# Kernel tuning notes

Hardware: AMD Instinct MI355X
Metric: run time of the kernel (lower is better)

Reference implementation:

```python
import jax, jax.numpy as jnp
import numpy as np

N_NODES = 50000
N_EDGES = 800000
N_GRAPHS = 256
DIMS = [64, 128, 256, 512]
GRU_H = 256


def _linit(key, shape, fan_in):
    lim = 1.0 / np.sqrt(fan_in)
    return jax.random.uniform(key, shape, jnp.float32, -lim, lim)


def setup_inputs() -> dict:
    key = jax.random.key(0)
    ks = jax.random.split(key, 24)
    x = jax.random.normal(ks[0], (N_NODES, DIMS[0]), jnp.float32)
    edge_index = jax.random.randint(ks[1], (2, N_EDGES), 0, N_NODES, jnp.int64)
    batch_idx = jnp.sort(jax.random.randint(ks[2], (N_NODES,), 0, N_GRAPHS, jnp.int64))
    inp = {"x": x, "edge_index": edge_index, "batch_idx": batch_idx}
    # GCN layer weights (stored [in, out]) and biases
    for i in range(3):
        inp[f"gcn_w{i}"] = _linit(ks[3 + i], (DIMS[i], DIMS[i + 1]), DIMS[i])
        inp[f"gcn_b{i}"] = jnp.zeros((DIMS[i + 1],), jnp.float32)
    # gate nn: Linear(512, 1)
    inp["gate_w"] = _linit(ks[6], (DIMS[3], 1), DIMS[3])
    inp["gate_b"] = jnp.zeros((1,), jnp.float32)
    # GRU: 2 layers, torch layout W_ih [3H, in], W_hh [3H, H]
    ins = [DIMS[3], GRU_H]
    for l in range(2):
        inp[f"gru_wih{l}"] = _linit(ks[7 + 4 * l], (3 * GRU_H, ins[l]), GRU_H)
        inp[f"gru_whh{l}"] = _linit(ks[8 + 4 * l], (3 * GRU_H, GRU_H), GRU_H)
        inp[f"gru_bih{l}"] = _linit(ks[9 + 4 * l], (3 * GRU_H,), GRU_H)
        inp[f"gru_bhh{l}"] = _linit(ks[10 + 4 * l], (3 * GRU_H,), GRU_H)
    # output proj: Linear(256, 512), torch layout [out, in]
    inp["proj_w"] = _linit(ks[15], (DIMS[3], GRU_H), GRU_H)
    inp["proj_b"] = jnp.zeros((DIMS[3],), jnp.float32)
    return inp


def _gcn_norm(edge_index, n_nodes):
    # add self-loops, symmetric normalization (PyG GCNConv default)
    loop = jnp.arange(n_nodes, dtype=edge_index.dtype)
    src = jnp.concatenate([edge_index[0], loop])
    dst = jnp.concatenate([edge_index[1], loop])
    deg = jax.ops.segment_sum(jnp.ones_like(dst, jnp.float32), dst, num_segments=n_nodes)
    dinv = jnp.where(deg > 0, jax.lax.rsqrt(jnp.maximum(deg, 1.0)), 0.0)
    norm = dinv[src] * dinv[dst]
    return src, dst, norm


def _gru_cell(xv, h, wih, whh, bih, bhh):
    gi = xv @ wih.T + bih
    gh = h @ whh.T + bhh
    ir, iz, inn = jnp.split(gi, 3, axis=-1)
    hr, hz, hn = jnp.split(gh, 3, axis=-1)
    r = jax.nn.sigmoid(ir + hr)
    z = jax.nn.sigmoid(iz + hz)
    n = jnp.tanh(inn + r * hn)
    return (1.0 - z) * n + z * h


def reference(x, edge_index, batch_idx,
              gcn_w0, gcn_b0, gcn_w1, gcn_b1, gcn_w2, gcn_b2,
              gate_w, gate_b,
              gru_wih0, gru_whh0, gru_bih0, gru_bhh0,
              gru_wih1, gru_whh1, gru_bih1, gru_bhh1,
              proj_w, proj_b):
    n = x.shape[0]
    src, dst, norm = _gcn_norm(edge_index, n)
    for w, b in ((gcn_w0, gcn_b0), (gcn_w1, gcn_b1), (gcn_w2, gcn_b2)):
        h = x @ w                                  # [N, out]
        msg = h[src] * norm[:, None]               # gather over edges
        x = jax.ops.segment_sum(msg, dst, num_segments=n) + b
        x = jax.nn.relu(x)
    # attentional aggregation: segment softmax over gate scores
    gate = (x @ gate_w + gate_b)[:, 0]             # [N]
    gmax = jax.ops.segment_max(gate, batch_idx, num_segments=N_GRAPHS)
    e = jnp.exp(gate - gmax[batch_idx])
    denom = jax.ops.segment_sum(e, batch_idx, num_segments=N_GRAPHS)
    alpha = e / denom[batch_idx]
    graph_emb = jax.ops.segment_sum(x * alpha[:, None], batch_idx, num_segments=N_GRAPHS)  # [G, 512]
    # 2-layer GRU with seq_len=1, h0=0
    h0 = jnp.zeros((N_GRAPHS, GRU_H), x.dtype)
    h1 = _gru_cell(graph_emb, h0, gru_wih0, gru_whh0, gru_bih0, gru_bhh0)
    h2 = _gru_cell(h1, h0, gru_wih1, gru_whh1, gru_bih1, gru_bhh1)
    return h2 @ proj_w.T + proj_b                  # [G, 512]
```

## Files before the change

kernel.cpp:

```cpp
#include <hip/hip_runtime.h>


#define N_GRAPHS 256
#define GRU_H 256
#define SCAN_CHUNK 2048

typedef __attribute__((ext_vector_type(8))) short short8;
typedef __attribute__((ext_vector_type(4))) float floatx4;

typedef unsigned short ushort_t;
typedef unsigned int uint_t;

__device__ __forceinline__ float bflo(uint_t u) { return __uint_as_float(u << 16); }
__device__ __forceinline__ float bfhi(uint_t u) { return __uint_as_float(u & 0xffff0000u); }
__device__ __forceinline__ uint_t f2bf(float f) {
    uint_t u = __float_as_uint(f);
    return (u + 0x7fffu + ((u >> 16) & 1u)) >> 16;
}
__device__ __forceinline__ uint_t pack2(float a, float b) {
    return f2bf(a) | (f2bf(b) << 16);
}


__global__ void k_hist(const int* __restrict__ dst, int* __restrict__ counts, int E) {
    int e = blockIdx.x * blockDim.x + threadIdx.x;
    if (e < E) atomicAdd(&counts[dst[e]], 1);
}

__global__ __launch_bounds__(256) void k_scan1(const int* __restrict__ counts,
                                               int* __restrict__ rowptr,
                                               int* __restrict__ bsums,
                                               float* __restrict__ dinv, int n) {
    int b = blockIdx.x, t = threadIdx.x;
    int base = b * SCAN_CHUNK + t * 8;
    int v[8];
    int s = 0;
#pragma unroll
    for (int j = 0; j < 8; ++j) {
        int i = base + j;
        int c = (i < n) ? counts[i] : 0;
        v[j] = s;
        s += c;
        if (i < n) dinv[i] = rsqrtf((float)(c + 1));
    }
    __shared__ int sd[256];
    sd[t] = s;
    __syncthreads();
    for (int off = 1; off < 256; off <<= 1) {
        int tmp = (t >= off) ? sd[t - off] : 0;
        __syncthreads();
        sd[t] += tmp;
        __syncthreads();
    }
    int texcl = sd[t] - s;
    if (t == 255) bsums[b] = sd[255];
#pragma unroll
    for (int j = 0; j < 8; ++j) {
        int i = base + j;
        if (i < n) rowptr[i] = texcl + v[j];
    }
}

__global__ void k_scan2(int* __restrict__ bsums, int nb, int* __restrict__ rowptr, int n) {
    if (threadIdx.x == 0 && blockIdx.x == 0) {
        int run = 0;
        for (int b = 0; b < nb; ++b) { int t = bsums[b]; bsums[b] = run; run += t; }
        rowptr[n] = run;
    }
}

__global__ __launch_bounds__(256) void k_scan3(int* __restrict__ rowptr,
                                               int* __restrict__ cursor,
                                               const int* __restrict__ bsums, int n) {
    int b = blockIdx.x, t = threadIdx.x;
    int base = b * SCAN_CHUNK + t * 8;
    int off = bsums[b];
#pragma unroll
    for (int j = 0; j < 8; ++j) {
        int i = base + j;
        if (i < n) { int r = rowptr[i] + off; rowptr[i] = r; cursor[i] = r; }
    }
}

__global__ void k_fill(const int* __restrict__ src, const int* __restrict__ dst,
                       int* __restrict__ cursor, int* __restrict__ col, int E) {
    int e = blockIdx.x * blockDim.x + threadIdx.x;
    if (e < E) {
        int pos = atomicAdd(&cursor[dst[e]], 1);
        col[pos] = src[e];
    }
}


__global__ void k_wt(const float* __restrict__ W, ushort_t* __restrict__ Wt,
                     int K, int Nout, int shift ) {
    int idx = blockIdx.x * blockDim.x + threadIdx.x;
    if (idx >= K * Nout) return;
    int k = idx >> shift;
    int n = idx & (Nout - 1);
    Wt[(size_t)n * K + k] = (ushort_t)f2bf(W[idx]);
}


__global__ void k_split(const float* __restrict__ src, ushort_t* __restrict__ hi,
                        ushort_t* __restrict__ lo, int L) {
    int i = blockIdx.x * blockDim.x + threadIdx.x;
    if (i >= L) return;
    float v = src[i];
    uint_t h = f2bf(v);
    hi[i] = (ushort_t)h;
    lo[i] = (ushort_t)f2bf(v - __uint_as_float(h << 16));
}


__global__ void k_prescale(const float4* __restrict__ x, const float* __restrict__ dinv,
                           uint4* __restrict__ xs, int N) {
    int idx = blockIdx.x * blockDim.x + threadIdx.x;
    int n = idx >> 3;
    if (n >= N) return;
    float dn = dinv[n];
    float4 v0 = x[idx * 2], v1 = x[idx * 2 + 1];
    uint4 o;
    o.x = pack2(v0.x * dn, v0.y * dn);
    o.y = pack2(v0.z * dn, v0.w * dn);
    o.z = pack2(v1.x * dn, v1.y * dn);
    o.w = pack2(v1.z * dn, v1.w * dn);
    xs[idx] = o;
}


__global__ void k_gather_bf16(const uint4* __restrict__ xs, const int* __restrict__ rp,
                              const int* __restrict__ col, const float* __restrict__ dinv,
                              uint4* __restrict__ agg, int N, int shift ) {
    int idx = blockIdx.x * blockDim.x + threadIdx.x;
    int n = idx >> shift;
    if (n >= N) return;
    int c = idx & ((1 << shift) - 1);
    int C8 = 1 << shift;
    int a = rp[n], b = rp[n + 1];
    uint4 u = xs[(size_t)n * C8 + c];
    float a0 = bflo(u.x), a1 = bfhi(u.x), a2 = bflo(u.y), a3 = bfhi(u.y);
    float a4 = bflo(u.z), a5 = bfhi(u.z), a6 = bflo(u.w), a7 = bfhi(u.w);
    for (int k = a; k < b; ++k) {
        uint4 v = xs[(size_t)col[k] * C8 + c];
        a0 += bflo(v.x); a1 += bfhi(v.x); a2 += bflo(v.y); a3 += bfhi(v.y);
        a4 += bflo(v.z); a5 += bfhi(v.z); a6 += bflo(v.w); a7 += bfhi(v.w);
    }
    float dn = dinv[n];
    uint4 o;
    o.x = pack2(a0 * dn, a1 * dn);
    o.y = pack2(a2 * dn, a3 * dn);
    o.z = pack2(a4 * dn, a5 * dn);
    o.w = pack2(a6 * dn, a7 * dn);
    agg[idx] = o;
}


__global__ __launch_bounds__(256) void k_gemm_mfma(
    const ushort_t* __restrict__ A, const ushort_t* __restrict__ Wt,
    const float* __restrict__ bias, const float* __restrict__ dinv,
    ushort_t* __restrict__ C, int M, int K, int Nout, int scale_out) {
    __shared__ ushort_t As[64 * 72];
    __shared__ ushort_t Bs[64 * 72];
    int tid = threadIdx.x;
    int wave = tid >> 6, lane = tid & 63;
    int quad = lane >> 4, lr = lane & 15;
    int wm = (wave & 1) * 32, wn = (wave >> 1) * 32;
    int bm = blockIdx.x * 64, bn = blockIdx.y * 64;

    floatx4 zero = {0.f, 0.f, 0.f, 0.f};
    floatx4 acc00 = zero, acc01 = zero, acc10 = zero, acc11 = zero;

    int r0 = tid >> 3,         ko0 = (tid & 7) * 8;
    int r1 = (tid + 256) >> 3, ko1 = ((tid + 256) & 7) * 8;

    for (int k0 = 0; k0 < K; k0 += 64) {
        int ar0 = min(bm + r0, M - 1);
        int ar1 = min(bm + r1, M - 1);
        uint4 av0 = *(const uint4*)(A + (size_t)ar0 * K + k0 + ko0);
        uint4 av1 = *(const uint4*)(A + (size_t)ar1 * K + k0 + ko1);
        uint4 bv0 = *(const uint4*)(Wt + (size_t)(bn + r0) * K + k0 + ko0);
        uint4 bv1 = *(const uint4*)(Wt + (size_t)(bn + r1) * K + k0 + ko1);
        __syncthreads();
        *(uint4*)&As[r0 * 72 + ko0] = av0;
        *(uint4*)&As[r1 * 72 + ko1] = av1;
        *(uint4*)&Bs[r0 * 72 + ko0] = bv0;
        *(uint4*)&Bs[r1 * 72 + ko1] = bv1;
        __syncthreads();
#pragma unroll
        for (int ks = 0; ks < 2; ++ks) {
            short8 af0 = *(short8*)&As[(wm + lr) * 72 + ks * 32 + quad * 8];
            short8 af1 = *(short8*)&As[(wm + 16 + lr) * 72 + ks * 32 + quad * 8];
            short8 bf0 = *(short8*)&Bs[(wn + lr) * 72 + ks * 32 + quad * 8];
            short8 bf1 = *(short8*)&Bs[(wn + 16 + lr) * 72 + ks * 32 + quad * 8];
            acc00 = __builtin_amdgcn_mfma_f32_16x16x32_bf16(af0, bf0, acc00, 0, 0, 0);
            acc01 = __builtin_amdgcn_mfma_f32_16x16x32_bf16(af0, bf1, acc01, 0, 0, 0);
            acc10 = __builtin_amdgcn_mfma_f32_16x16x32_bf16(af1, bf0, acc10, 0, 0, 0);
            acc11 = __builtin_amdgcn_mfma_f32_16x16x32_bf16(af1, bf1, acc11, 0, 0, 0);
        }
    }

#pragma unroll
    for (int mi = 0; mi < 2; ++mi) {
#pragma unroll
        for (int ni = 0; ni < 2; ++ni) {
            floatx4 acc = (mi == 0) ? (ni == 0 ? acc00 : acc01)
                                    : (ni == 0 ? acc10 : acc11);
            int col = bn + wn + ni * 16 + lr;
            float bcol = bias[col];
#pragma unroll
            for (int r = 0; r < 4; ++r) {
                int row = bm + wm + mi * 16 + quad * 4 + r;
                if (row < M) {
                    float v = acc[r] + bcol;
                    v = fmaxf(v, 0.0f);
                    if (scale_out) v *= dinv[row];
                    C[(size_t)row * Nout + col] = (ushort_t)f2bf(v);
                }
            }
        }
    }
}


__global__ __launch_bounds__(256) void k_gemm3(
    const ushort_t* __restrict__ Ahi, const ushort_t* __restrict__ Alo,
    const ushort_t* __restrict__ Whi, const ushort_t* __restrict__ Wlo,
    const float* __restrict__ bias, float* __restrict__ C,
    int M, int K, int Nout) {
    __shared__ ushort_t AsH[64 * 72];
    __shared__ ushort_t AsL[64 * 72];
    __shared__ ushort_t BsH[64 * 72];
    __shared__ ushort_t BsL[64 * 72];
    int tid = threadIdx.x;
    int wave = tid >> 6, lane = tid & 63;
    int quad = lane >> 4, lr = lane & 15;
    int wm = (wave & 1) * 32, wn = (wave >> 1) * 32;
    int bm = blockIdx.x * 64, bn = blockIdx.y * 64;

    floatx4 zero = {0.f, 0.f, 0.f, 0.f};
    floatx4 acc00 = zero, acc01 = zero, acc10 = zero, acc11 = zero;

    int r0 = tid >> 3,         ko0 = (tid & 7) * 8;
    int r1 = (tid + 256) >> 3, ko1 = ((tid + 256) & 7) * 8;

    for (int k0 = 0; k0 < K; k0 += 64) {
        int ar0 = min(bm + r0, M - 1);
        int ar1 = min(bm + r1, M - 1);
        size_t a0o = (size_t)ar0 * K + k0 + ko0, a1o = (size_t)ar1 * K + k0 + ko1;
        size_t b0o = (size_t)(bn + r0) * K + k0 + ko0, b1o = (size_t)(bn + r1) * K + k0 + ko1;
        uint4 ah0 = *(const uint4*)(Ahi + a0o), ah1 = *(const uint4*)(Ahi + a1o);
        uint4 al0 = *(const uint4*)(Alo + a0o), al1 = *(const uint4*)(Alo + a1o);
        uint4 bh0 = *(const uint4*)(Whi + b0o), bh1 = *(const uint4*)(Whi + b1o);
        uint4 bl0 = *(const uint4*)(Wlo + b0o), bl1 = *(const uint4*)(Wlo + b1o);
        __syncthreads();
        *(uint4*)&AsH[r0 * 72 + ko0] = ah0; *(uint4*)&AsH[r1 * 72 + ko1] = ah1;
        *(uint4*)&AsL[r0 * 72 + ko0] = al0; *(uint4*)&AsL[r1 * 72 + ko1] = al1;
        *(uint4*)&BsH[r0 * 72 + ko0] = bh0; *(uint4*)&BsH[r1 * 72 + ko1] = bh1;
        *(uint4*)&BsL[r0 * 72 + ko0] = bl0; *(uint4*)&BsL[r1 * 72 + ko1] = bl1;
        __syncthreads();
#pragma unroll
        for (int ks = 0; ks < 2; ++ks) {
            int a0i = (wm + lr) * 72 + ks * 32 + quad * 8;
            int a1i = (wm + 16 + lr) * 72 + ks * 32 + quad * 8;
            int b0i = (wn + lr) * 72 + ks * 32 + quad * 8;
            int b1i = (wn + 16 + lr) * 72 + ks * 32 + quad * 8;
            short8 afh0 = *(short8*)&AsH[a0i], afh1 = *(short8*)&AsH[a1i];
            short8 afl0 = *(short8*)&AsL[a0i], afl1 = *(short8*)&AsL[a1i];
            short8 bfh0 = *(short8*)&BsH[b0i], bfh1 = *(short8*)&BsH[b1i];
            short8 bfl0 = *(short8*)&BsL[b0i], bfl1 = *(short8*)&BsL[b1i];
            acc00 = __builtin_amdgcn_mfma_f32_16x16x32_bf16(afh0, bfh0, acc00, 0, 0, 0);
            acc00 = __builtin_amdgcn_mfma_f32_16x16x32_bf16(afh0, bfl0, acc00, 0, 0, 0);
            acc00 = __builtin_amdgcn_mfma_f32_16x16x32_bf16(afl0, bfh0, acc00, 0, 0, 0);
            acc01 = __builtin_amdgcn_mfma_f32_16x16x32_bf16(afh0, bfh1, acc01, 0, 0, 0);
            acc01 = __builtin_amdgcn_mfma_f32_16x16x32_bf16(afh0, bfl1, acc01, 0, 0, 0);
            acc01 = __builtin_amdgcn_mfma_f32_16x16x32_bf16(afl0, bfh1, acc01, 0, 0, 0);
            acc10 = __builtin_amdgcn_mfma_f32_16x16x32_bf16(afh1, bfh0, acc10, 0, 0, 0);
            acc10 = __builtin_amdgcn_mfma_f32_16x16x32_bf16(afh1, bfl0, acc10, 0, 0, 0);
            acc10 = __builtin_amdgcn_mfma_f32_16x16x32_bf16(afl1, bfh0, acc10, 0, 0, 0);
            acc11 = __builtin_amdgcn_mfma_f32_16x16x32_bf16(afh1, bfh1, acc11, 0, 0, 0);
            acc11 = __builtin_amdgcn_mfma_f32_16x16x32_bf16(afh1, bfl1, acc11, 0, 0, 0);
            acc11 = __builtin_amdgcn_mfma_f32_16x16x32_bf16(afl1, bfh1, acc11, 0, 0, 0);
        }
    }

#pragma unroll
    for (int mi = 0; mi < 2; ++mi) {
#pragma unroll
        for (int ni = 0; ni < 2; ++ni) {
            floatx4 acc = (mi == 0) ? (ni == 0 ? acc00 : acc01)
                                    : (ni == 0 ? acc10 : acc11);
            int col = bn + wn + ni * 16 + lr;
            float bcol = bias ? bias[col] : 0.0f;
#pragma unroll
            for (int r = 0; r < 4; ++r) {
                int row = bm + wm + mi * 16 + quad * 4 + r;
                if (row < M)
                    C[(size_t)row * Nout + col] = acc[r] + bcol;
            }
        }
    }
}


__global__ void k_gru_ep(const float* __restrict__ gi, const float* __restrict__ bih,
                         const float* __restrict__ bhh,
                         ushort_t* __restrict__ hhi, ushort_t* __restrict__ hlo, int G) {
    int idx = blockIdx.x * blockDim.x + threadIdx.x;
    int g = idx >> 8, j = idx & 255;
    if (g >= G) return;
    const float* row = gi + (size_t)g * 768;
    float ir = row[j]       + bih[j]       + bhh[j];
    float iz = row[j + 256] + bih[j + 256] + bhh[j + 256];
    float in = row[j + 512] + bih[j + 512];
    float r = 1.0f / (1.0f + expf(-ir));
    float z = 1.0f / (1.0f + expf(-iz));
    float nn = tanhf(in + r * bhh[j + 512]);
    float h = (1.0f - z) * nn;
    uint_t hi = f2bf(h);
    hhi[idx] = (ushort_t)hi;
    hlo[idx] = (ushort_t)f2bf(h - __uint_as_float(hi << 16));
}


__global__ void k_gate(const uint4* __restrict__ x, const float4* __restrict__ gw,
                       const float* __restrict__ gb, float* __restrict__ gate, int N) {
    int gid = blockIdx.x * blockDim.x + threadIdx.x;
    int wave = gid >> 6;
    int lane = gid & 63;
    if (wave >= N) return;
    uint4 u = x[(size_t)wave * 64 + lane];
    float4 w0 = gw[lane * 2], w1 = gw[lane * 2 + 1];
    float acc = bflo(u.x) * w0.x + bfhi(u.x) * w0.y + bflo(u.y) * w0.z + bfhi(u.y) * w0.w
              + bflo(u.z) * w1.x + bfhi(u.z) * w1.y + bflo(u.w) * w1.z + bfhi(u.w) * w1.w;
#pragma unroll
    for (int off = 32; off > 0; off >>= 1) acc += __shfl_down(acc, off, 64);
    if (lane == 0) gate[wave] = acc + gb[0];
}


__global__ void k_gstart(const int* __restrict__ batch, int* __restrict__ gstart,
                         int N, int G) {
    int g = blockIdx.x * blockDim.x + threadIdx.x;
    if (g > G) return;
    if (g == G) { gstart[G] = N; return; }
    int lo = 0, hi = N;
    while (lo < hi) {
        int mid = (lo + hi) >> 1;
        if (batch[mid] < g) lo = mid + 1; else hi = mid;
    }
    gstart[g] = lo;
}


__global__ __launch_bounds__(256) void k_softmax_emb(
    const uint_t* __restrict__ x , const float* __restrict__ gate,
    const int* __restrict__ gstart, float* __restrict__ emb) {
    int g = blockIdx.x;
    int s = gstart[g], e = gstart[g + 1];
    __shared__ float red[256];
    __shared__ float sal[256];
    int tid = threadIdx.x;
    float m = -INFINITY;
    for (int i = s + tid; i < e; i += 256) m = fmaxf(m, gate[i]);
    red[tid] = m; __syncthreads();
    for (int off = 128; off > 0; off >>= 1) {
        if (tid < off) red[tid] = fmaxf(red[tid], red[tid + off]);
        __syncthreads();
    }
    m = red[0]; __syncthreads();
    float ssum = 0.f;
    for (int i = s + tid; i < e; i += 256) ssum += expf(gate[i] - m);
    red[tid] = ssum; __syncthreads();
    for (int off = 128; off > 0; off >>= 1) {
        if (tid < off) red[tid] += red[tid + off];
        __syncthreads();
    }
    float denom = red[0];
    float inv = (denom > 0.f) ? 1.0f / denom : 0.0f;
    float acc0 = 0.f, acc1 = 0.f;
    for (int base = s; base < e; base += 256) {
        int i = base + tid;
        __syncthreads();
        sal[tid] = (i < e) ? expf(gate[i] - m) * inv : 0.0f;
        __syncthreads();
        int cnt = min(256, e - base);
        for (int k = 0; k < cnt; ++k) {
            float a = sal[k];
            uint_t u = x[(size_t)(base + k) * 256 + tid];
            acc0 += a * bflo(u);
            acc1 += a * bfhi(u);
        }
    }
    emb[(size_t)g * 512 + tid * 2]     = acc0;
    emb[(size_t)g * 512 + tid * 2 + 1] = acc1;
}


extern "C" void kernel_launch(void* const* d_in, const int* in_sizes, int n_in,
                              void* d_out, int out_size, void* d_ws, size_t ws_size,
                              hipStream_t stream) {
    const float* x       = (const float*)d_in[0];
    const int*   ei      = (const int*)d_in[1];
    const int*   batch   = (const int*)d_in[2];
    const float* w0      = (const float*)d_in[3];
    const float* b0      = (const float*)d_in[4];
    const float* w1      = (const float*)d_in[5];
    const float* b1      = (const float*)d_in[6];
    const float* w2      = (const float*)d_in[7];
    const float* b2      = (const float*)d_in[8];
    const float* gate_w  = (const float*)d_in[9];
    const float* gate_b  = (const float*)d_in[10];
    const float* wih0    = (const float*)d_in[11];
    const float* bih0    = (const float*)d_in[13];
    const float* bhh0    = (const float*)d_in[14];
    const float* wih1    = (const float*)d_in[15];
    const float* bih1    = (const float*)d_in[17];
    const float* bhh1    = (const float*)d_in[18];
    const float* pw      = (const float*)d_in[19];
    const float* pb      = (const float*)d_in[20];
    float* out = (float*)d_out;

    const int N = in_sizes[2];
    const int E = in_sizes[1] / 2;
    const int G = N_GRAPHS;

    char* base = (char*)d_ws;
    size_t off = 0;
    auto alloc = [&](size_t bytes) -> char* {
        char* p = base + off;
        off = (off + bytes + 255) & ~(size_t)255;
        return p;
    };
    ushort_t* bufA  = (ushort_t*)alloc((size_t)N * 512 * 2);
    ushort_t* bufB  = (ushort_t*)alloc((size_t)N * 512 * 2);
    float* dinv     = (float*)alloc((size_t)N * 4);
    float* gateArr  = (float*)alloc((size_t)N * 4);
    int*   counts   = (int*)alloc((size_t)(N + 1) * 4);
    int*   cursor   = (int*)alloc((size_t)(N + 1) * 4);
    int*   rowptr   = (int*)alloc((size_t)(N + 1) * 4);
    int*   bsums    = (int*)alloc((size_t)256 * 4);
    int*   col      = (int*)alloc((size_t)E * 4);
    int*   gstart   = (int*)alloc((size_t)(G + 1) * 4);
    float* emb      = (float*)alloc((size_t)G * 512 * 4);
    ushort_t* wt0   = (ushort_t*)alloc((size_t)128 * 64 * 2);
    ushort_t* wt1   = (ushort_t*)alloc((size_t)256 * 128 * 2);
    ushort_t* wt2   = (ushort_t*)alloc((size_t)512 * 256 * 2);
    ushort_t* ih0H  = (ushort_t*)alloc((size_t)768 * 512 * 2);
    ushort_t* ih0L  = (ushort_t*)alloc((size_t)768 * 512 * 2);
    ushort_t* ih1H  = (ushort_t*)alloc((size_t)768 * 256 * 2);
    ushort_t* ih1L  = (ushort_t*)alloc((size_t)768 * 256 * 2);
    ushort_t* pwH   = (ushort_t*)alloc((size_t)512 * 256 * 2);
    ushort_t* pwL   = (ushort_t*)alloc((size_t)512 * 256 * 2);
    ushort_t* embH  = (ushort_t*)alloc((size_t)G * 512 * 2);
    ushort_t* embL  = (ushort_t*)alloc((size_t)G * 512 * 2);
    ushort_t* h1H   = (ushort_t*)alloc((size_t)G * 256 * 2);
    ushort_t* h1L   = (ushort_t*)alloc((size_t)G * 256 * 2);
    ushort_t* h2H   = (ushort_t*)alloc((size_t)G * 256 * 2);
    ushort_t* h2L   = (ushort_t*)alloc((size_t)G * 256 * 2);
    float* gi       = (float*)alloc((size_t)G * 768 * 4);
    (void)ws_size; (void)n_in; (void)out_size;

    const int* src = ei;
    const int* dst = ei + E;

    const int nb = (N + SCAN_CHUNK - 1) / SCAN_CHUNK;

    hipMemsetAsync(counts, 0, (size_t)(N + 1) * 4, stream);
    k_hist<<<(E + 255) / 256, 256, 0, stream>>>(dst, counts, E);
    k_scan1<<<nb, 256, 0, stream>>>(counts, rowptr, bsums, dinv, N);
    k_scan2<<<1, 64, 0, stream>>>(bsums, nb, rowptr, N);
    k_scan3<<<nb, 256, 0, stream>>>(rowptr, cursor, bsums, N);
    k_fill<<<(E + 255) / 256, 256, 0, stream>>>(src, dst, cursor, col, E);
    k_wt<<<(64 * 128 + 255) / 256, 256, 0, stream>>>(w0, wt0, 64, 128, 7);
    k_wt<<<(128 * 256 + 255) / 256, 256, 0, stream>>>(w1, wt1, 128, 256, 8);
    k_wt<<<(256 * 512 + 255) / 256, 256, 0, stream>>>(w2, wt2, 256, 512, 9);
    k_split<<<(768 * 512 + 255) / 256, 256, 0, stream>>>(wih0, ih0H, ih0L, 768 * 512);
    k_split<<<(768 * 256 + 255) / 256, 256, 0, stream>>>(wih1, ih1H, ih1L, 768 * 256);
    k_split<<<(512 * 256 + 255) / 256, 256, 0, stream>>>(pw, pwH, pwL, 512 * 256);

    int mBlocks = (N + 63) / 64;

    k_prescale<<<(N * 8 + 255) / 256, 256, 0, stream>>>((const float4*)x, dinv, (uint4*)bufA, N);
    k_gather_bf16<<<(N * 8 + 255) / 256, 256, 0, stream>>>((const uint4*)bufA, rowptr, col, dinv, (uint4*)bufB, N, 3);
    k_gemm_mfma<<<dim3(mBlocks, 2), 256, 0, stream>>>(bufB, wt0, b0, dinv, bufA, N, 64, 128, 1);

    k_gather_bf16<<<(N * 16 + 255) / 256, 256, 0, stream>>>((const uint4*)bufA, rowptr, col, dinv, (uint4*)bufB, N, 4);
    k_gemm_mfma<<<dim3(mBlocks, 4), 256, 0, stream>>>(bufB, wt1, b1, dinv, bufA, N, 128, 256, 1);

    k_gather_bf16<<<(N * 32 + 255) / 256, 256, 0, stream>>>((const uint4*)bufA, rowptr, col, dinv, (uint4*)bufB, N, 5);
    k_gemm_mfma<<<dim3(mBlocks, 8), 256, 0, stream>>>(bufB, wt2, b2, dinv, bufA, N, 256, 512, 0);

    k_gate<<<(N * 64 + 255) / 256, 256, 0, stream>>>((const uint4*)bufA, (const float4*)gate_w, gate_b, gateArr, N);
    k_gstart<<<1, 512, 0, stream>>>(batch, gstart, N, G);
    k_softmax_emb<<<G, 256, 0, stream>>>((const uint_t*)bufA, gateArr, gstart, emb);

    k_split<<<(G * 512 + 255) / 256, 256, 0, stream>>>(emb, embH, embL, G * 512);
    k_gemm3<<<dim3(G / 64, 12), 256, 0, stream>>>(embH, embL, ih0H, ih0L, nullptr, gi, G, 512, 768);
    k_gru_ep<<<G, 256, 0, stream>>>(gi, bih0, bhh0, h1H, h1L, G);

    k_gemm3<<<dim3(G / 64, 12), 256, 0, stream>>>(h1H, h1L, ih1H, ih1L, nullptr, gi, G, 256, 768);
    k_gru_ep<<<G, 256, 0, stream>>>(gi, bih1, bhh1, h2H, h2L, G);

    k_gemm3<<<dim3(G / 64, 8), 256, 0, stream>>>(h2H, h2L, pwH, pwL, pb, out, G, 256, 512);
}
```

Before: 487.1 us.

## Unroll edge gather loop for MLP and enlarge GEMM tiles to 128x128

The CSR gather kernel now loads 8 (then 4) column indices and neighbor rows at a time before accumulating, so more independent memory loads are in flight per thread. The MFMA GEMM grows its block tile from 64x64 to 128x128, with each wave computing a 64x64 subtile through a 4x4 grid of MFMA accumulators, which gives more data reuse per shared-memory load. The cost is higher register and LDS use per block and fewer blocks, which may lower occupancy.

Measured after the change: 551.9 us. 1.13x slower.

```diff
diff --git a/kernel.cpp b/kernel.cpp
--- a/kernel.cpp
+++ b/kernel.cpp
@@ -129,6 +129,13 @@
 }
 
 
+__device__ __forceinline__ void acc8(float& a0, float& a1, float& a2, float& a3,
+                                     float& a4, float& a5, float& a6, float& a7,
+                                     const uint4& v) {
+    a0 += bflo(v.x); a1 += bfhi(v.x); a2 += bflo(v.y); a3 += bfhi(v.y);
+    a4 += bflo(v.z); a5 += bfhi(v.z); a6 += bflo(v.w); a7 += bfhi(v.w);
+}
+
 __global__ void k_gather_bf16(const uint4* __restrict__ xs, const int* __restrict__ rp,
                               const int* __restrict__ col, const float* __restrict__ dinv,
                               uint4* __restrict__ agg, int N, int shift ) {
@@ -141,10 +148,32 @@
     uint4 u = xs[(size_t)n * C8 + c];
     float a0 = bflo(u.x), a1 = bfhi(u.x), a2 = bflo(u.y), a3 = bfhi(u.y);
     float a4 = bflo(u.z), a5 = bfhi(u.z), a6 = bflo(u.w), a7 = bfhi(u.w);
-    for (int k = a; k < b; ++k) {
+    int k = a;
+    for (; k + 8 <= b; k += 8) {
+        int ci[8];
+#pragma unroll
+        for (int j = 0; j < 8; ++j) ci[j] = col[k + j];
+        uint4 v[8];
+#pragma unroll
+        for (int j = 0; j < 8; ++j) v[j] = xs[(size_t)ci[j] * C8 + c];
+#pragma unroll
+        for (int j = 0; j < 8; ++j)
+            acc8(a0, a1, a2, a3, a4, a5, a6, a7, v[j]);
+    }
+    for (; k + 4 <= b; k += 4) {
+        int ci[4];
+#pragma unroll
+        for (int j = 0; j < 4; ++j) ci[j] = col[k + j];
+        uint4 v[4];
+#pragma unroll
+        for (int j = 0; j < 4; ++j) v[j] = xs[(size_t)ci[j] * C8 + c];
+#pragma unroll
+        for (int j = 0; j < 4; ++j)
+            acc8(a0, a1, a2, a3, a4, a5, a6, a7, v[j]);
+    }
+    for (; k < b; ++k) {
         uint4 v = xs[(size_t)col[k] * C8 + c];
-        a0 += bflo(v.x); a1 += bfhi(v.x); a2 += bflo(v.y); a3 += bfhi(v.y);
-        a4 += bflo(v.z); a5 += bfhi(v.z); a6 += bflo(v.w); a7 += bfhi(v.w);
+        acc8(a0, a1, a2, a3, a4, a5, a6, a7, v);
     }
     float dn = dinv[n];
     uint4 o;
@@ -160,59 +189,63 @@
     const ushort_t* __restrict__ A, const ushort_t* __restrict__ Wt,
     const float* __restrict__ bias, const float* __restrict__ dinv,
     ushort_t* __restrict__ C, int M, int K, int Nout, int scale_out) {
-    __shared__ ushort_t As[64 * 72];
-    __shared__ ushort_t Bs[64 * 72];
+    __shared__ ushort_t As[128 * 72];
+    __shared__ ushort_t Bs[128 * 72];
     int tid = threadIdx.x;
     int wave = tid >> 6, lane = tid & 63;
     int quad = lane >> 4, lr = lane & 15;
-    int wm = (wave & 1) * 32, wn = (wave >> 1) * 32;
-    int bm = blockIdx.x * 64, bn = blockIdx.y * 64;
-
-    floatx4 zero = {0.f, 0.f, 0.f, 0.f};
-    floatx4 acc00 = zero, acc01 = zero, acc10 = zero, acc11 = zero;
-
-    int r0 = tid >> 3,         ko0 = (tid & 7) * 8;
-    int r1 = (tid + 256) >> 3, ko1 = ((tid + 256) & 7) * 8;
+    int wm = (wave & 1) * 64, wn = (wave >> 1) * 64;
+    int bm = blockIdx.x * 128, bn = blockIdx.y * 128;
+
+    floatx4 acc[4][4] = {};
 
     for (int k0 = 0; k0 < K; k0 += 64) {
-        int ar0 = min(bm + r0, M - 1);
-        int ar1 = min(bm + r1, M - 1);
-        uint4 av0 = *(const uint4*)(A + (size_t)ar0 * K + k0 + ko0);
-        uint4 av1 = *(const uint4*)(A + (size_t)ar1 * K + k0 + ko1);
-        uint4 bv0 = *(const uint4*)(Wt + (size_t)(bn + r0) * K + k0 + ko0);
-        uint4 bv1 = *(const uint4*)(Wt + (size_t)(bn + r1) * K + k0 + ko1);
-        __syncthreads();
-        *(uint4*)&As[r0 * 72 + ko0] = av0;
-        *(uint4*)&As[r1 * 72 + ko1] = av1;
-        *(uint4*)&Bs[r0 * 72 + ko0] = bv0;
-        *(uint4*)&Bs[r1 * 72 + ko1] = bv1;
+        uint4 av[4], bv[4];
+#pragma unroll
+        for (int i = 0; i < 4; ++i) {
+            int ch = tid + i * 256;
+            int row = ch >> 3, ko = (ch & 7) * 8;
+            int ar = min(bm + row, M - 1);
+            av[i] = *(const uint4*)(A + (size_t)ar * K + k0 + ko);
+            bv[i] = *(const uint4*)(Wt + (size_t)(bn + row) * K + k0 + ko);
+        }
+        __syncthreads();
+#pragma unroll
+        for (int i = 0; i < 4; ++i) {
+            int ch = tid + i * 256;
+            int row = ch >> 3, ko = (ch & 7) * 8;
+            *(uint4*)&As[row * 72 + ko] = av[i];
+            *(uint4*)&Bs[row * 72 + ko] = bv[i];
+        }
         __syncthreads();
 #pragma unroll
         for (int ks = 0; ks < 2; ++ks) {
-            short8 af0 = *(short8*)&As[(wm + lr) * 72 + ks * 32 + quad * 8];
-            short8 af1 = *(short8*)&As[(wm + 16 + lr) * 72 + ks * 32 + quad * 8];
-            short8 bf0 = *(short8*)&Bs[(wn + lr) * 72 + ks * 32 + quad * 8];
-            short8 bf1 = *(short8*)&Bs[(wn + 16 + lr) * 72 + ks * 32 + quad * 8];
-            acc00 = __builtin_amdgcn_mfma_f32_16x16x32_bf16(af0, bf0, acc00, 0, 0, 0);
-            acc01 = __builtin_amdgcn_mfma_f32_16x16x32_bf16(af0, bf1, acc01, 0, 0, 0);
-            acc10 = __builtin_amdgcn_mfma_f32_16x16x32_bf16(af1, bf0, acc10, 0, 0, 0);
-            acc11 = __builtin_amdgcn_mfma_f32_16x16x32_bf16(af1, bf1, acc11, 0, 0, 0);
-        }
-    }
-
-#pragma unroll
-    for (int mi = 0; mi < 2; ++mi) {
-#pragma unroll
-        for (int ni = 0; ni < 2; ++ni) {
-            floatx4 acc = (mi == 0) ? (ni == 0 ? acc00 : acc01)
-                                    : (ni == 0 ? acc10 : acc11);
+            short8 af[4], bf[4];
+#pragma unroll
+            for (int i = 0; i < 4; ++i) {
+                af[i] = *(short8*)&As[(wm + i * 16 + lr) * 72 + ks * 32 + quad * 8];
+                bf[i] = *(short8*)&Bs[(wn + i * 16 + lr) * 72 + ks * 32 + quad * 8];
+            }
+#pragma unroll
+            for (int mi = 0; mi < 4; ++mi)
+#pragma unroll
+                for (int ni = 0; ni < 4; ++ni)
+                    acc[mi][ni] = __builtin_amdgcn_mfma_f32_16x16x32_bf16(
+                        af[mi], bf[ni], acc[mi][ni], 0, 0, 0);
+        }
+    }
+
+#pragma unroll
+    for (int mi = 0; mi < 4; ++mi) {
+#pragma unroll
+        for (int ni = 0; ni < 4; ++ni) {
             int col = bn + wn + ni * 16 + lr;
             float bcol = bias[col];
 #pragma unroll
             for (int r = 0; r < 4; ++r) {
                 int row = bm + wm + mi * 16 + quad * 4 + r;
                 if (row < M) {
-                    float v = acc[r] + bcol;
+                    float v = acc[mi][ni][r] + bcol;
                     v = fmaxf(v, 0.0f);
                     if (scale_out) v *= dinv[row];
                     C[(size_t)row * Nout + col] = (ushort_t)f2bf(v);
@@ -479,17 +512,17 @@
     k_split<<<(768 * 256 + 255) / 256, 256, 0, stream>>>(wih1, ih1H, ih1L, 768 * 256);
     k_split<<<(512 * 256 + 255) / 256, 256, 0, stream>>>(pw, pwH, pwL, 512 * 256);
 
-    int mBlocks = (N + 63) / 64;
+    int mBlocks128 = (N + 127) / 128;
 
     k_prescale<<<(N * 8 + 255) / 256, 256, 0, stream>>>((const float4*)x, dinv, (uint4*)bufA, N);
     k_gather_bf16<<<(N * 8 + 255) / 256, 256, 0, stream>>>((const uint4*)bufA, rowptr, col, dinv, (uint4*)bufB, N, 3);
-    k_gemm_mfma<<<dim3(mBlocks, 2), 256, 0, stream>>>(bufB, wt0, b0, dinv, bufA, N, 64, 128, 1);
+    k_gemm_mfma<<<dim3(mBlocks128, 1), 256, 0, stream>>>(bufB, wt0, b0, dinv, bufA, N, 64, 128, 1);
 
     k_gather_bf16<<<(N * 16 + 255) / 256, 256, 0, stream>>>((const uint4*)bufA, rowptr, col, dinv, (uint4*)bufB, N, 4);
-    k_gemm_mfma<<<dim3(mBlocks, 4), 256, 0, stream>>>(bufB, wt1, b1, dinv, bufA, N, 128, 256, 1);
+    k_gemm_mfma<<<dim3(mBlocks128, 2), 256, 0, stream>>>(bufB, wt1, b1, dinv, bufA, N, 128, 256, 1);
 
     k_gather_bf16<<<(N * 32 + 255) / 256, 256, 0, stream>>>((const uint4*)bufA, rowptr, col, dinv, (uint4*)bufB, N, 5);
-    k_gemm_mfma<<<dim3(mBlocks, 8), 256, 0, stream>>>(bufB, wt2, b2, dinv, bufA, N, 256, 512, 0);
+    k_gemm_mfma<<<dim3(mBlocks128, 4), 256, 0, stream>>>(bufB, wt2, b2, dinv, bufA, N, 256, 512, 0);
 
     k_gate<<<(N * 64 + 255) / 256, 256, 0, stream>>>((const uint4*)bufA, (const float4*)gate_w, gate_b, gateArr, N);
     k_gstart<<<1, 512, 0, stream>>>(batch, gstart, N, G);
```
